# Performance work log

Measured on AMD Instinct MI355X. Metric: run time of the kernel, lower is better.

## Reference

```python
import jax, jax.numpy as jnp
import numpy as np

B, N, DE, DX, H = 16, 128, 4, 11, 128
LAMBDA_BOUND = 1e-4


def setup_inputs() -> dict:
    key = jax.random.key(0)
    k1, k2, k3, k4, k5 = jax.random.split(key, 5)
    # symmetric sparse random graph (avg degree ~12) so the Laplacian has a generic spectrum
    m = jax.random.bernoulli(k1, 0.1, (B, N, N))
    adj = jnp.logical_or(m, jnp.swapaxes(m, 1, 2))
    adj = adj & ~jnp.eye(N, dtype=bool)[None]
    A = jax.random.normal(k2, (B, N, N, DE), dtype=jnp.float32) * adj[..., None].astype(jnp.float32)
    X = jax.random.normal(k3, (B, N, DX), dtype=jnp.float32)
    nodemask = jnp.zeros((B, N), dtype=bool)
    W_edge = jax.random.normal(k4, (DE, H), dtype=jnp.float32) * 0.1
    b_edge = jnp.zeros((H,), dtype=jnp.float32)
    W_x = jax.random.normal(k5, (DX, H), dtype=jnp.float32) * 0.1
    b_x = jnp.zeros((H,), dtype=jnp.float32)
    mu = jnp.linspace(0.0, 2.0, H, dtype=jnp.float32)       # RBF centers
    inv_sigma = jnp.full((H,), 4.0, dtype=jnp.float32)       # RBF inverse widths
    return {"A": A, "X": X, "nodemask": nodemask, "W_edge": W_edge, "b_edge": b_edge,
            "W_x": W_x, "b_x": b_x, "mu": mu, "inv_sigma": inv_sigma}


def reference(A, X, nodemask, W_edge, b_edge, W_x, b_x, mu, inv_sigma):
    # edge embedding (qm9 path: Linear(4, hiddim))
    eA = jnp.einsum('bnmd,dh->bnmh', A, W_edge) + b_edge            # (b,n,n,h)
    # adjacency / degree
    adj = jnp.any(A != 0, axis=-1).astype(A.dtype)                   # (b,n,n)
    D = jnp.sum(adj, axis=-1)                                        # (b,n)
    # normalized Laplacian
    n = adj.shape[1]
    L = D[:, :, None] * jnp.eye(n, dtype=A.dtype) - adj
    tD = jax.lax.rsqrt(jnp.maximum(D, 1.0))
    L = tD[:, None, :] * L * tD[:, :, None]
    # batched symmetric eigendecomposition (eval mode: no permutation / noise)
    Lambda, U = jnp.linalg.eigh(L)                                   # (b,n), (b,n,n)
    Lambda = Lambda[:, 1:]                                           # drop trivial eigenpair
    U = U[:, :, 1:]                                                  # (b,n,n-1)
    # node embedding (Linear(11, hiddim)) + mask
    Xh = jnp.einsum('bnd,dh->bnh', X, W_x) + b_x
    Xh = jnp.where(nodemask[..., None], 0.0, Xh)
    # eigen masking
    Lambdamask = jnp.abs(Lambda) < LAMBDA_BOUND                      # (b,n-1)
    U = jnp.where(Lambdamask[:, None, :], 0.0, U)
    U = jnp.where(nodemask[:, :, None], 0.0, U)
    Lambda = jnp.sqrt(jax.nn.relu(Lambda))
    # Gaussian RBF expansion of eigenvalues -> (b,n-1,h)
    LambdaEmb = jnp.exp(-jnp.square((Lambda[..., None] - mu) * inv_sigma))
    # mask edge embeddings on padded nodes
    eA = jnp.where(nodemask[:, None, :, None], 0.0, eA)
    eA = jnp.where(nodemask[:, :, None, None], 0.0, eA)
    # node-edge combine: (b,n,m,h) x (b,m,l) -> (b,n,l,h)
    Uc = jnp.einsum('bnmd,bml->bnld', eA, U)
    return (LambdaEmb, Lambdamask, Uc, Xh, nodemask)
```

## Files before the change

### kernel.cpp

```cpp
#include <hip/hip_runtime.h>

#define NBATCH 16
#define NN 128
#define NH 128
#define NL 127
#define NDX 11
#define NDE 4
#define LDA 132
#define LDB 129
#define LDT 132
#define WS_STRIDE 66560

#define OFF_AREF 0
#define OFF_Q0   16384
#define OFF_Q1   32768
#define OFF_S    49152
#define OFF_DV   65536
#define OFF_EV   65664
#define OFF_TAU  65792
#define OFF_ORG  65920
#define OFF_META 66048

#define EPS32 5.9604645e-8f
#define EPS232 3.5527137e-15f
#define SAFMIN32 1.17549435e-38f

__device__ __forceinline__ float ssign_(float a, float b) {
  return (b >= 0.0f) ? fabsf(a) : -fabsf(a);
}
__device__ __forceinline__ float slapy2_(float x, float y) {
  float ax = fabsf(x), ay = fabsf(y);
  float w = fmaxf(ax, ay), z = fminf(ax, ay);
  if (z == 0.0f) return w;
  float q = z / w;
  return w * sqrtf(1.0f + q * q);
}

__device__ __forceinline__ float rdl(float v, int src) {
  return __int_as_float(__builtin_amdgcn_readlane(__float_as_int(v), src));
}

__device__ void slartg_(float f, float g, float* c, float* s, float* r) {
  if (g == 0.0f) { *c = 1.0f; *s = 0.0f; *r = f; }
  else if (f == 0.0f) { *c = 0.0f; *s = (g >= 0.0f) ? 1.0f : -1.0f; *r = fabsf(g); }
  else {
    float d = sqrtf(f * f + g * g);
    d = (f >= 0.0f) ? d : -d;
    *c = f / d; *s = g / d; *r = d;
  }
}

__device__ void slaev2_(float a, float b, float c0, float* rt1, float* rt2,
                        float* cs1, float* sn1) {
  float sm = a + c0, df = a - c0, adf = fabsf(df), tb = b + b, ab = fabsf(tb);
  float acmx, acmn;
  if (fabsf(a) > fabsf(c0)) { acmx = a; acmn = c0; } else { acmx = c0; acmn = a; }
  float rt;
  if (adf > ab) { float q = ab / adf; rt = adf * sqrtf(1.0f + q * q); }
  else if (adf < ab) { float q = adf / ab; rt = ab * sqrtf(1.0f + q * q); }
  else rt = ab * sqrtf(2.0f);
  int sgn1;
  if (sm < 0.0f) { *rt1 = 0.5f * (sm - rt); sgn1 = -1; *rt2 = (acmx / *rt1) * acmn - (b / *rt1) * b; }
  else if (sm > 0.0f) { *rt1 = 0.5f * (sm + rt); sgn1 = 1; *rt2 = (acmx / *rt1) * acmn - (b / *rt1) * b; }
  else { *rt1 = 0.5f * rt; *rt2 = -0.5f * rt; sgn1 = 1; }
  int sgn2; float cs;
  if (df >= 0.0f) { cs = df + rt; sgn2 = 1; } else { cs = df - rt; sgn2 = -1; }
  float acs = fabsf(cs);
  if (acs > ab) { float ct = -tb / cs; *sn1 = 1.0f / sqrtf(1.0f + ct * ct); *cs1 = ct * (*sn1); }
  else {
    if (ab == 0.0f) { *cs1 = 1.0f; *sn1 = 0.0f; }
    else { float tn = -cs / tb; *cs1 = 1.0f / sqrtf(1.0f + tn * tn); *sn1 = tn * (*cs1); }
  }
  if (sgn1 == sgn2) { float tn = *cs1; *cs1 = -(*sn1); *sn1 = tn; }
}

__global__ __launch_bounds__(1024) void k_tridiag(const float* __restrict__ A_in,
                                                  float* __restrict__ wsG) {
  const int b = blockIdx.x, t = threadIdx.x;
  float* Aref = wsG + (size_t)b * WS_STRIDE;
  float* dv = Aref + OFF_DV;
  float* ev = Aref + OFF_EV;
  float* tg = Aref + OFF_TAU;
  float* og = Aref + OFF_ORG;
  extern __shared__ float As[];
  __shared__ unsigned int maskp[128][8];
  __shared__ unsigned int Dp[128][8];
  __shared__ unsigned long long adj0_[128], adj1_[128];
  __shared__ float Dd_[128], tDs_[128];
  __shared__ float d_[128], e_[128], tau_[128];
  __shared__ alignas(16) float v_[128];
  __shared__ alignas(16) float w_[128];
  __shared__ float pmat[8][128];
  __shared__ alignas(16) float red_[16];

  const int wid = t >> 6;
  const int lane = t & 63;
  {
    const int r8 = t >> 3, s8 = t & 7;
    const float4* Arow = (const float4*)(A_in + (size_t)(b * 128 + r8) * 128 * 4);
    unsigned int mloc = 0; unsigned int cnt = 0;
    const int m0 = s8 * 16;
    #pragma unroll 4
    for (int mm = 0; mm < 16; ++mm) {
      float4 a = Arow[m0 + mm];
      if (a.x != 0.f || a.y != 0.f || a.z != 0.f || a.w != 0.f) { mloc |= 1u << mm; cnt++; }
    }
    maskp[r8][s8] = mloc; Dp[r8][s8] = cnt;
  }
  __syncthreads();
  if (t < 128) {
    unsigned long long b0 = 0ull, b1 = 0ull; unsigned int D = 0;
    #pragma unroll
    for (int s = 0; s < 4; ++s) { b0 |= (unsigned long long)maskp[t][s] << (16 * s); D += Dp[t][s]; }
    #pragma unroll
    for (int s = 0; s < 4; ++s) { b1 |= (unsigned long long)maskp[t][s + 4] << (16 * s); D += Dp[t][s + 4]; }
    adj0_[t] = b0; adj1_[t] = b1;
    float Df = (float)D;
    Dd_[t] = Df;
    tDs_[t] = 1.0f / sqrtf(fmaxf(Df, 1.0f));
  }
  __syncthreads();
  for (int idx = t; idx < 16384; idx += 1024) {
    int r = idx >> 7, c = idx & 127;
    if (c <= r) {
      float adj = (float)((c < 64 ? (adj0_[r] >> c) : (adj1_[r] >> (c - 64))) & 1ull);
      float Lrc = ((c == r) ? Dd_[r] : 0.0f) - adj;
      float val = (tDs_[c] * Lrc) * tDs_[r];
      As[r * LDA + c] = val;
      As[c * LDA + r] = val;
    }
  }
  __syncthreads();

  const int rmv = t & 127;
  const int smv = t >> 7;
  const int ucg = t & 31;
  const int urs = t >> 5;

  for (int i = 0; i < 127; ++i) {
    const int lo = i + 1;
    float xi = 0.0f;
    float part = 0.0f;
    if (t < 128) {
      xi = As[t * LDA + i];
      if (t >= i + 2) part = xi * xi;
    }
    if (wid < 2) {
      #pragma unroll
      for (int m = 1; m < 64; m <<= 1) part += __shfl_xor(part, m);
      if (lane == 0) red_[wid] = part;
    }
    __syncthreads();
    float xnorm2 = red_[0] + red_[1];
    float alpha = As[lo * LDA + i];
    float beta, taui, scal;
    if (xnorm2 == 0.0f) { taui = 0.0f; beta = alpha; scal = 0.0f; }
    else {
      float xn = sqrtf(xnorm2);
      beta = -ssign_(slapy2_(alpha, xn), alpha);
      taui = (beta - alpha) / beta;
      scal = 1.0f / (alpha - beta);
    }
    if (t == 0) { e_[i] = beta; tau_[i] = taui; }
    if (taui != 0.0f) {
      if (t < 128) {
        float vv = 0.0f;
        if (t == lo) vv = 1.0f;
        else if (t > lo) { vv = xi * scal; As[t * LDA + i] = vv; }
        v_[t] = vv;
      }
      __syncthreads();
      const int c0 = smv * 16;
      float acc = 0.0f;
      if (c0 + 15 >= lo && rmv >= lo) {
        const float4* Ar = (const float4*)&As[rmv * LDA + c0];
        const float4* Vr = (const float4*)&v_[c0];
        #pragma unroll
        for (int k = 0; k < 4; ++k) {
          float4 a = Ar[k], v4 = Vr[k];
          acc += a.x * v4.x + a.y * v4.y + a.z * v4.z + a.w * v4.w;
        }
      }
      pmat[smv][rmv] = acc;
      __syncthreads();
      if (t < 128) {
        float pv = 0.0f;
        #pragma unroll
        for (int s = 0; s < 8; ++s) pv += pmat[s][t];
        float wt = taui * pv;
        w_[t] = wt;
        float p2 = v_[t] * wt;
        #pragma unroll
        for (int m = 1; m < 64; m <<= 1) p2 += __shfl_xor(p2, m);
        if (lane == 0) red_[wid] = p2;
      }
      __syncthreads();
      float a2 = -0.5f * taui * (red_[0] + red_[1]);
      const int uc0 = ucg * 4;
      if (uc0 + 3 >= lo) {
        float4 vc = *(const float4*)&v_[uc0];
        float4 wc = *(const float4*)&w_[uc0];
        float pcx = wc.x + a2 * vc.x;
        float pcy = wc.y + a2 * vc.y;
        float pcz = wc.z + a2 * vc.z;
        float pcw = wc.w + a2 * vc.w;
        if (uc0 < lo) {
          if (uc0 + 0 < lo) { vc.x = 0.f; pcx = 0.f; }
          if (uc0 + 1 < lo) { vc.y = 0.f; pcy = 0.f; }
          if (uc0 + 2 < lo) { vc.z = 0.f; pcz = 0.f; }
        }
        #pragma unroll
        for (int k = 0; k < 4; ++k) {
          int r = urs + 32 * k;
          if (r >= lo) {
            float vr = v_[r];
            float pr = w_[r] + a2 * vr;
            float4 a = *(const float4*)&As[r * LDA + uc0];
            a.x -= vr * pcx + pr * vc.x;
            a.y -= vr * pcy + pr * vc.y;
            a.z -= vr * pcz + pr * vc.z;
            a.w -= vr * pcw + pr * vc.w;
            *(float4*)&As[r * LDA + uc0] = a;
          }
        }
      }
    }
    __syncthreads();
  }
  if (t < 128) d_[t] = As[t * LDA + t];
  __syncthreads();

  {
    float mx = 0.0f;
    if (t < 128) mx = fabsf(d_[t]);
    if (t < 127) mx = fmaxf(mx, fabsf(e_[t]));
    if (wid < 2) {
      #pragma unroll
      for (int m = 1; m < 64; m <<= 1) mx = fmaxf(mx, __shfl_xor(mx, m));
      if (lane == 0) red_[wid] = mx;
    }
    __syncthreads();
  }
  float orgnrm = fmaxf(red_[0], red_[1]);
  if (orgnrm == 0.0f) orgnrm = 1.0f;
  float invnrm = 1.0f / orgnrm;
  if (t < 128) d_[t] *= invnrm;
  if (t < 127) e_[t] *= invnrm;
  __syncthreads();
  if (t == 0) {
    for (int bm = 16; bm < 128; bm += 16) {
      float ae = fabsf(e_[bm - 1]);
      d_[bm - 1] -= ae; d_[bm] -= ae;
    }
  }
  __syncthreads();
  for (int idx = t; idx < 16384; idx += 1024)
    Aref[idx] = As[(idx >> 7) * LDA + (idx & 127)];
  if (t < 128) { dv[t] = d_[t]; tg[t] = tau_[t]; }
  if (t < 127) ev[t] = e_[t];
  if (t == 0) og[0] = orgnrm;
}

__global__ __launch_bounds__(64) void k_leaves(float* __restrict__ wsG) {
  int b = blockIdx.x >> 3, lf = blockIdx.x & 7;
  float* base = wsG + (size_t)b * WS_STRIDE;
  float* Qg = base + OFF_Q0;
  float* dv = base + OFF_DV;
  float* ev = base + OFF_EV;
  const int ln = threadIdx.x;
  __shared__ float zsh[16 * 17];

  const int n = 16;
  float dreg = (ln < 16) ? dv[lf * 16 + ln] : 0.f;
  float ereg = (ln < 15) ? ev[lf * 16 + ln] : 0.f;
  float csreg = 0.f, snreg = 0.f;
  float zr[16];
  #pragma unroll
  for (int c = 0; c < 16; ++c) zr[c] = (ln == c) ? 1.0f : 0.0f;

  {
    const float eps = EPS32, eps2 = EPS232, safmin = SAFMIN32;
    int nmaxit = n * 30, jtot = 0;
    int l1 = 0;
    while (l1 <= n - 1) {
      if (l1 > 0 && ln == l1 - 1) ereg = 0.0f;
      int m;
      for (m = l1; m <= n - 2; ++m) {
        float tst = fabsf(rdl(ereg, m));
        if (tst == 0.0f) break;
        if (tst <= (sqrtf(fabsf(rdl(dreg, m))) * sqrtf(fabsf(rdl(dreg, m + 1)))) * eps) {
          if (ln == m) ereg = 0.0f;
          break;
        }
      }
      int l = l1, lend = m;
      l1 = m + 1;
      if (lend == l) continue;
      {
        float an = 0.0f;
        for (int i = l; i <= lend; ++i) an = fmaxf(an, fabsf(rdl(dreg, i)));
        for (int i = l; i <= lend - 1; ++i) an = fmaxf(an, fabsf(rdl(ereg, i)));
        if (an == 0.0f) continue;
      }
      if (fabsf(rdl(dreg, lend)) < fabsf(rdl(dreg, l))) { int tsw = l; l = lend; lend = tsw; }
      if (lend > l) {
        while (true) {
          int m2;
          if (l != lend) {
            for (m2 = l; m2 <= lend - 1; ++m2) {
              float em = rdl(ereg, m2);
              float tst = em * em;
              if (tst <= (eps2 * fabsf(rdl(dreg, m2))) * fabsf(rdl(dreg, m2 + 1)) + safmin) break;
            }
          } else m2 = lend;
          if (m2 < lend && ln == m2) ereg = 0.0f;
          float p = rdl(dreg, l);
          if (m2 == l) { l++; if (l <= lend) continue; else break; }
          if (m2 == l + 1) {
            float rt1, rt2, c, s;
            slaev2_(rdl(dreg, l), rdl(ereg, l), rdl(dreg, l + 1), &rt1, &rt2, &c, &s);
            #pragma unroll
            for (int j = 0; j < 15; ++j) {
              if (j == l) {
                float t1 = zr[j + 1];
                zr[j + 1] = c * t1 - s * zr[j];
                zr[j] = s * t1 + c * zr[j];
              }
            }
            if (ln == l) { dreg = rt1; ereg = 0.0f; }
            if (ln == l + 1) dreg = rt2;
            l += 2; if (l <= lend) continue; else break;
          }
          if (jtot == nmaxit) break;
          jtot++;
          float g = (rdl(dreg, l + 1) - p) / (2.0f * rdl(ereg, l));
          float r = slapy2_(g, 1.0f);
          g = rdl(dreg, m2) - p + rdl(ereg, l) / (g + ssign_(r, g));
          float s = 1.0f, c = 1.0f; p = 0.0f;
          for (int i = m2 - 1; i >= l; --i) {
            float ei = rdl(ereg, i);
            float f = s * ei, bb = c * ei;
            slartg_(g, f, &c, &s, &r);
            if (i != m2 - 1 && ln == i + 1) ereg = r;
            g = rdl(dreg, i + 1) - p;
            r = (rdl(dreg, i) - g) * s + 2.0f * c * bb;
            p = s * r;
            if (ln == i + 1) dreg = g + p;
            g = c * r - bb;
            if (ln == i) { csreg = c; snreg = -s; }
          }
          #pragma unroll
          for (int j = 14; j >= 0; --j) {
            if (j <= m2 - 1 && j >= l) {
              float cj = rdl(csreg, j), sj = rdl(snreg, j);
              float t1 = zr[j + 1];
              zr[j + 1] = cj * t1 - sj * zr[j];
              zr[j] = sj * t1 + cj * zr[j];
            }
          }
          if (ln == l) { dreg = dreg - p; ereg = g; }
        }
      } else {
        while (true) {
          int m2;
          if (l != lend) {
            for (m2 = l; m2 >= lend + 1; --m2) {
              float em = rdl(ereg, m2 - 1);
              float tst = em * em;
              if (tst <= (eps2 * fabsf(rdl(dreg, m2))) * fabsf(rdl(dreg, m2 - 1)) + safmin) break;
            }
          } else m2 = lend;
          if (m2 > lend && ln == m2 - 1) ereg = 0.0f;
          float p = rdl(dreg, l);
          if (m2 == l) { l--; if (l >= lend) continue; else break; }
          if (m2 == l - 1) {
            float rt1, rt2, c, s;
            slaev2_(rdl(dreg, l - 1), rdl(ereg, l - 1), rdl(dreg, l), &rt1, &rt2, &c, &s);
            #pragma unroll
            for (int j = 0; j < 15; ++j) {
              if (j == l - 1) {
                float t1 = zr[j + 1];
                zr[j + 1] = c * t1 - s * zr[j];
                zr[j] = s * t1 + c * zr[j];
              }
            }
            if (ln == l - 1) { dreg = rt1; ereg = 0.0f; }
            if (ln == l) dreg = rt2;
            l -= 2; if (l >= lend) continue; else break;
          }
          if (jtot == nmaxit) break;
          jtot++;
          float g = (rdl(dreg, l - 1) - p) / (2.0f * rdl(ereg, l - 1));
          float r = slapy2_(g, 1.0f);
          g = rdl(dreg, m2) - p + rdl(ereg, l - 1) / (g + ssign_(r, g));
          float s = 1.0f, c = 1.0f; p = 0.0f;
          for (int i = m2; i <= l - 1; ++i) {
            float ei = rdl(ereg, i);
            float f = s * ei, bb = c * ei;
            slartg_(g, f, &c, &s, &r);
            if (i != m2 && ln == i - 1) ereg = r;
            g = rdl(dreg, i) - p;
            r = (rdl(dreg, i + 1) - g) * s + 2.0f * c * bb;
            p = s * r;
            if (ln == i) dreg = g + p;
            g = c * r - bb;
            if (ln == i) { csreg = c; snreg = s; }
          }
          #pragma unroll
          for (int j = 0; j <= 14; ++j) {
            if (j >= m2 && j <= l - 1) {
              float cj = rdl(csreg, j), sj = rdl(snreg, j);
              float t1 = zr[j + 1];
              zr[j + 1] = cj * t1 - sj * zr[j];
              zr[j] = sj * t1 + cj * zr[j];
            }
          }
          if (ln == l) dreg = dreg - p;
          if (ln == l - 1) ereg = g;
        }
      }
    }
  }

  if (ln < 16) {
    #pragma unroll
    for (int c = 0; c < 16; ++c) zsh[ln * 17 + c] = zr[c];
  }
  __syncthreads();
  for (int ii = 1; ii <= n - 1; ++ii) {
    int i = ii - 1, k = i;
    float p = rdl(dreg, i);
    for (int j = ii; j <= n - 1; ++j) {
      float dj = rdl(dreg, j);
      if (dj < p) { k = j; p = dj; }
    }
    if (k != i) {
      float di = rdl(dreg, i);
      if (ln == k) dreg = di;
      if (ln == i) dreg = p;
      if (ln < 16) {
        float t1 = zsh[ln * 17 + i];
        zsh[ln * 17 + i] = zsh[ln * 17 + k];
        zsh[ln * 17 + k] = t1;
      }
    }
  }
  __syncthreads();
  if (ln < 16) dv[lf * 16 + ln] = dreg;
  {
    const int bo = (lf >> 1) * 32;
    const int cofs = (lf & 1) * 16;
    for (int idx = ln; idx < 16 * 32; idx += 64) {
      int rr = idx >> 5, c = idx & 31;
      int cl = c - cofs;
      float v = (cl >= 0 && cl < 16) ? zsh[rr * 17 + cl] : 0.f;
      Qg[(size_t)(lf * 16 + rr) * 128 + bo + c] = v;
    }
  }
}

template <int LVL>
__global__ __launch_bounds__(1024) void k_mergeA(float* __restrict__ wsG, int qoff) {
  constexpr int sh = 2 - LVL;
  constexpr int nm = 32 << LVL;
  constexpr int LPR = 1024 / nm;
  constexpr int NCH = nm / LPR;
  int b = blockIdx.x >> sh;
  int mg = blockIdx.x & ((1 << sh) - 1);
  int bo = mg * nm, n1 = nm >> 1, n = nm;
  const int t = threadIdx.x;
  float* base = wsG + (size_t)b * WS_STRIDE;
  float* Qin = base + qoff;
  float* dvg = base + OFF_DV;
  float* evg = base + OFF_EV;
  float* Sg  = base + OFF_S;
  int* meta = (int*)(base + OFF_META);
  int* undG = meta; int* idxpG = meta + 128; int* finG = meta + 256; int* KfG = meta + 384;

  __shared__ float d_[128], z_[128], dl_[128], w_[128], zh_[128], lam_[128], tauv_[128], dnew_[128];
  __shared__ int srt_[128], indxp_[128], und_[128], anc_[128], fin_[128];
  __shared__ int gp_[128], gq_[128];
  __shared__ float gc_[128], gs_[128];
  __shared__ int sci[4];

  if (t < n) d_[t] = dvg[bo + t];
  float rho_in = evg[bo + n1 - 1];
  if (t < n) {
    float zv = (t < n1) ? Qin[(size_t)(bo + n1 - 1) * 128 + bo + t]
                        : Qin[(size_t)(bo + n1) * 128 + bo + t];
    if (rho_in < 0.0f && t >= n1) zv = -zv;
    z_[t] = zv * 0.70710678f;
  }
  __syncthreads();
  float rho = fabsf(2.0f * rho_in);
  if (t == 0) {
    int i1 = 0, i2 = n1, k = 0;
    while (i1 < n1 && i2 < n) {
      if (d_[i1] <= d_[i2]) srt_[k++] = i1++; else srt_[k++] = i2++;
    }
    while (i1 < n1) srt_[k++] = i1++;
    while (i2 < n) srt_[k++] = i2++;
    float zmax = 0.0f, dmax = 0.0f;
    for (int i = 0; i < n; ++i) {
      zmax = fmaxf(zmax, fabsf(z_[i]));
      dmax = fmaxf(dmax, fabsf(d_[i]));
    }
    float tol = 8.0f * EPS32 * fmaxf(dmax, zmax);
    int K = 0, k2 = n, full = 0, ngiv = 0;
    if (rho * zmax <= tol) full = 1;
    else {
      int pj = -1, jj = 0;
      for (; jj < n; ++jj) {
        int nj = srt_[jj];
        if (rho * fabsf(z_[nj]) <= tol) { k2--; indxp_[k2] = nj; }
        else { pj = nj; break; }
      }
      if (pj < 0) full = 1;
      else {
        for (jj = jj + 1; jj < n; ++jj) {
          int nj = srt_[jj];
          if (rho * fabsf(z_[nj]) <= tol) { k2--; indxp_[k2] = nj; }
          else {
            float s = z_[pj], c = z_[nj];
            float tauq = slapy2_(c, s);
            float tdf = d_[nj] - d_[pj];
            c /= tauq; s = -s / tauq;
            if (fabsf(tdf * c * s) <= tol) {
              z_[nj] = tauq; z_[pj] = 0.0f;
              gp_[ngiv] = pj; gq_[ngiv] = nj; gc_[ngiv] = c; gs_[ngiv] = s; ngiv++;
              float tt2 = d_[pj] * c * c + d_[nj] * s * s;
              d_[nj] = d_[pj] * s * s + d_[nj] * c * c;
              d_[pj] = tt2;
              k2--;
              int pos = k2;
              while (pos + 1 <= n - 1 && d_[pj] < d_[indxp_[pos + 1]]) {
                indxp_[pos] = indxp_[pos + 1]; pos++;
              }
              indxp_[pos] = pj;
              pj = nj;
            } else {
              dl_[K] = d_[pj]; w_[K] = z_[pj]; und_[K] = pj; K++;
              pj = nj;
            }
          }
        }
        dl_[K] = d_[pj]; w_[K] = z_[pj]; und_[K] = pj; K++;
      }
    }
    sci[0] = K; sci[1] = full; sci[2] = ngiv;
  }
  __syncthreads();
  int K = sci[0], full = sci[1], ngiv = sci[2];
  if (!full) {
    if (t < n) {
      size_t rowoff = (size_t)(bo + t) * 128 + bo;
      for (int g = 0; g < ngiv; ++g) {
        float c = gc_[g], s = gs_[g];
        float xq = Qin[rowoff + gp_[g]], yq = Qin[rowoff + gq_[g]];
        Qin[rowoff + gp_[g]] = c * xq + s * yq;
        Qin[rowoff + gq_[g]] = c * yq - s * xq;
      }
    }
    const int j = t / LPR;
    const int sub = t % LPR;
    const bool act = (j < K);
    float dl_loc[NCH], w2_loc[NCH];
    float tauj_reg = 0.0f; float da_reg = 0.0f;
    if (act) {
      #pragma unroll
      for (int k = 0; k < NCH; ++k) {
        int i = sub + k * LPR;
        if (i < K) { dl_loc[k] = dl_[i]; float wi = w_[i]; w2_loc[k] = rho * wi * wi; }
        else { dl_loc[k] = 3.0e38f; w2_loc[k] = 0.0f; }
      }
      float zs = 0.0f;
      #pragma unroll
      for (int k = 0; k < NCH; ++k) zs += w2_loc[k];
      #pragma unroll
      for (int m = 1; m < LPR; m <<= 1) zs += __shfl_xor(zs, m);
      int a; float lo2, hi2;
      if (j < K - 1) {
        float dj = dl_[j];
        float tm = 0.5f * (dl_[j + 1] - dj);
        float fm = 0.0f;
        #pragma unroll
        for (int k = 0; k < NCH; ++k) fm += w2_loc[k] / ((dl_loc[k] - dj) - tm);
        #pragma unroll
        for (int m = 1; m < LPR; m <<= 1) fm += __shfl_xor(fm, m);
        fm += 1.0f;
        if (fm >= 0.0f) { a = j; lo2 = 0.0f; hi2 = tm; }
        else { a = j + 1; lo2 = -tm; hi2 = 0.0f; }
      } else { a = K - 1; lo2 = 0.0f; hi2 = zs + 1e-30f; }
      float da = dl_[a];
      float sdl[NCH];
      #pragma unroll
      for (int k = 0; k < NCH; ++k) sdl[k] = dl_loc[k] - da;
      for (int it2 = 0; it2 < 48; ++it2) {
        float tc = 0.5f * (lo2 + hi2);
        float f = 0.0f;
        #pragma unroll
        for (int k = 0; k < NCH; ++k) f += w2_loc[k] / (sdl[k] - tc);
        #pragma unroll
        for (int m = 1; m < LPR; m <<= 1) f += __shfl_xor(f, m);
        f += 1.0f;
        if (f >= 0.0f) hi2 = tc; else lo2 = tc;
      }
      tauj_reg = 0.5f * (lo2 + hi2);
      da_reg = da;
      if (sub == 0) { lam_[j] = da + tauj_reg; tauv_[j] = tauj_reg; anc_[j] = a; }
    }
    __syncthreads();
    if (act) {
      float di = dl_[j];
      float pp = 1.0f;
      #pragma unroll
      for (int k = 0; k < NCH; ++k) {
        int jj = sub + k * LPR;
        if (jj < K && jj != j) {
          float delta_ij = (di - dl_[anc_[jj]]) - tauv_[jj];
          pp *= delta_ij / (di - dl_[jj]);
        }
      }
      #pragma unroll
      for (int m = 1; m < LPR; m <<= 1) pp *= __shfl_xor(pp, m);
      if (sub == 0) {
        float lead = (di - da_reg) - tauj_reg;
        float acc = lead * pp;
        zh_[j] = ssign_(sqrtf(fmaxf(-acc, 0.0f)), w_[j]);
      }
    }
    __syncthreads();
    if (act) {
      float sv[NCH]; float nrm = 0.0f;
      #pragma unroll
      for (int k = 0; k < NCH; ++k) {
        int i = sub + k * LPR;
        float s = 0.0f;
        if (i < K) s = zh_[i] / ((dl_loc[k] - da_reg) - tauj_reg);
        sv[k] = s; nrm += s * s;
      }
      #pragma unroll
      for (int m = 1; m < LPR; m <<= 1) nrm += __shfl_xor(nrm, m);
      nrm = 1.0f / sqrtf(nrm);
      float* scol = Sg + bo + j;
      #pragma unroll
      for (int k = 0; k < NCH; ++k) {
        int i = sub + k * LPR;
        if (i < K) scol[(size_t)(bo + i) * 128] = sv[k] * nrm;
      }
    }
    if (t == 0) {
      for (int jj = 0; jj < K; ++jj) dnew_[jj] = lam_[jj];
      for (int m = 0; m < n - K; ++m) dnew_[K + m] = d_[indxp_[n - 1 - m]];
      int i1 = 0, i2 = K, k = 0;
      while (i1 < K && i2 < n) { if (dnew_[i1] <= dnew_[i2]) fin_[k++] = i1++; else fin_[k++] = i2++; }
      while (i1 < K) fin_[k++] = i1++;
      while (i2 < n) fin_[k++] = i2++;
    }
    __syncthreads();
    if (t < n) {
      dvg[bo + t] = dnew_[fin_[t]];
      idxpG[bo + t] = indxp_[t];
      finG[bo + t] = fin_[t];
    }
    if (t < K) undG[bo + t] = und_[t];
    if (t == 0) KfG[mg] = K;
  } else {
    if (t < n) {
      dvg[bo + t] = d_[srt_[t]];
      idxpG[bo + t] = srt_[n - 1 - t];
      finG[bo + t] = t;
    }
    if (t == 0) KfG[mg] = 0;
  }
}

__global__ __launch_bounds__(256) void k_mergeB(float* __restrict__ wsG, int lvl,
                                                int qinoff, int qoutoff) {
  int b = blockIdx.x >> 2;
  int rblk = blockIdx.x & 3;
  int rbase = rblk * 32;
  int nm = 32 << lvl;
  int ln2 = 5 + lvl;
  int mg = rbase >> ln2;
  int bo = mg * nm, n = nm;
  const int t = threadIdx.x;
  float* base = wsG + (size_t)b * WS_STRIDE;
  const float* Qin = base + qinoff;
  float* Qout = base + qoutoff;
  const float* Sg = base + OFF_S;
  const int* meta = (const int*)(base + OFF_META);
  const int* undG = meta; const int* idxpG = meta + 128;
  const int* finG = meta + 256; const int* KfG = meta + 384;

  extern __shared__ float lds[];
  float* QT = lds;
  float* QC = QT + 32 * LDB;
  float* WT = QC + 32 * LDB;
  float* ST = WT + 32 * LDB;
  __shared__ int und_l[128], idxp_l[128], fin_l[128];
  __shared__ int Ksh;

  if (t == 0) Ksh = KfG[mg];
  if (t < n) { und_l[t] = undG[bo + t]; idxp_l[t] = idxpG[bo + t]; fin_l[t] = finG[bo + t]; }
  for (int idx = t; idx < 32 * n; idx += 256) {
    int r = idx >> ln2, c = idx & (n - 1);
    QT[r * LDB + c] = Qin[(size_t)(rbase + r) * 128 + bo + c];
  }
  __syncthreads();
  int K = Ksh;
  for (int idx = t; idx < (K << 7); idx += 256) {
    int k = idx >> 7, j = idx & 127;
    ST[k * LDB + j] = Sg[(size_t)(bo + k) * 128 + bo + j];
  }
  for (int r = 0; r < 32; ++r)
    if (t < K) QC[r * LDB + t] = QT[r * LDB + und_l[t]];
  __syncthreads();
  for (int idx = t; idx < 32 * n; idx += 256) {
    int r = idx >> ln2, j = idx & (n - 1);
    float v;
    if (j < K) {
      float a0 = 0.f, a1 = 0.f, a2 = 0.f, a3 = 0.f;
      int k = 0;
      for (; k + 3 < K; k += 4) {
        a0 += QC[r * LDB + k]     * ST[k * LDB + j];
        a1 += QC[r * LDB + k + 1] * ST[(k + 1) * LDB + j];
        a2 += QC[r * LDB + k + 2] * ST[(k + 2) * LDB + j];
        a3 += QC[r * LDB + k + 3] * ST[(k + 3) * LDB + j];
      }
      for (; k < K; ++k) a0 += QC[r * LDB + k] * ST[k * LDB + j];
      v = (a0 + a1) + (a2 + a3);
    } else {
      v = QT[r * LDB + idxp_l[n - 1 - (j - K)]];
    }
    WT[r * LDB + j] = v;
  }
  __syncthreads();
  for (int idx = t; idx < 32 * 128; idx += 256) {
    int r = idx >> 7, c = idx & 127;
    int cl = c - bo;
    float v = 0.f;
    if (cl >= 0 && cl < n) v = WT[r * LDB + fin_l[cl]];
    Qout[(size_t)(rbase + r) * 128 + c] = v;
  }
}

__global__ __launch_bounds__(1024) void k_back(
    float* __restrict__ wsG, const unsigned char* __restrict__ nodemask,
    const float* __restrict__ mu, const float* __restrict__ isg,
    float* __restrict__ wsUt, float* __restrict__ wsLam,
    float* __restrict__ outEmb, float* __restrict__ outLmask) {
  const int b = blockIdx.x, t = threadIdx.x;
  float* base = wsG + (size_t)b * WS_STRIDE;
  float* Qg = base + OFF_Q1;
  float* dvg = base + OFF_DV;
  float* tg = base + OFF_TAU;
  float* og = base + OFF_ORG;
  extern __shared__ float lds[];
  float* At = lds;
  float* Qt = lds + 128 * LDT;
  __shared__ float d_[128], tau_[128];
  __shared__ unsigned char nm_[128];

  float orgnrm = og[0];
  for (int idx = t; idx < 16384; idx += 1024) {
    int r = idx >> 7, c = idx & 127;
    At[c * LDT + r] = base[idx];
    Qt[c * LDT + r] = Qg[idx];
  }
  if (t < 128) {
    d_[t] = dvg[t] * orgnrm;
    tau_[t] = tg[t];
    nm_[t] = nodemask[b * 128 + t];
  }
  __syncthreads();

  const int w = t >> 6, l = t & 63;
  const int cidx = l & 7, sg = l >> 3;
  const int c = w * 8 + cidx;
  float q[16];
  #pragma unroll
  for (int k = 0; k < 4; ++k) {
    float4 v = *(const float4*)&Qt[c * LDT + 4 * sg + 32 * k];
    q[4 * k + 0] = v.x; q[4 * k + 1] = v.y; q[4 * k + 2] = v.z; q[4 * k + 3] = v.w;
  }
  for (int i = 126; i >= 0; --i) {
    float taui = tau_[i];
    if (taui == 0.0f) continue;
    const int lo = i + 1;
    float a[16];
    float dot = 0.0f;
    #pragma unroll
    for (int k = 0; k < 4; ++k) {
      if (32 * k + 31 >= lo) {
        float4 av = *(const float4*)&At[i * LDT + 4 * sg + 32 * k];
        {
          int r = 4 * sg + 32 * k;
          float aj;
          aj = (r == lo) ? 1.0f : ((r > lo) ? av.x : 0.0f); a[4*k+0] = aj; dot += aj * q[4*k+0]; r++;
          aj = (r == lo) ? 1.0f : ((r > lo) ? av.y : 0.0f); a[4*k+1] = aj; dot += aj * q[4*k+1]; r++;
          aj = (r == lo) ? 1.0f : ((r > lo) ? av.z : 0.0f); a[4*k+2] = aj; dot += aj * q[4*k+2]; r++;
          aj = (r == lo) ? 1.0f : ((r > lo) ? av.w : 0.0f); a[4*k+3] = aj; dot += aj * q[4*k+3];
        }
      }
    }
    dot += __shfl_xor(dot, 8);
    dot += __shfl_xor(dot, 16);
    dot += __shfl_xor(dot, 32);
    float wv = taui * dot;
    #pragma unroll
    for (int k = 0; k < 4; ++k) {
      if (32 * k + 31 >= lo) {
        q[4*k+0] -= a[4*k+0] * wv;
        q[4*k+1] -= a[4*k+1] * wv;
        q[4*k+2] -= a[4*k+2] * wv;
        q[4*k+3] -= a[4*k+3] * wv;
      }
    }
  }
  #pragma unroll
  for (int k = 0; k < 4; ++k) {
    float4 v;
    v.x = q[4*k+0]; v.y = q[4*k+1]; v.z = q[4*k+2]; v.w = q[4*k+3];
    *(float4*)&Qt[c * LDT + 4 * sg + 32 * k] = v;
  }
  __syncthreads();

  if (t < NL) {
    float lam = d_[t + 1];
    wsLam[b * NL + t] = lam;
    outLmask[b * NL + t] = (fabsf(lam) < 1e-4f) ? 1.f : 0.f;
  }
  for (int idx = t; idx < NL * 128; idx += 1024) {
    int ll = idx >> 7, nn2 = idx & 127;
    float lam = d_[ll + 1];
    float vv = Qt[(ll + 1) * LDT + nn2];
    if (fabsf(lam) < 1e-4f || nm_[nn2]) vv = 0.f;
    wsUt[(size_t)(b * NL + ll) * 128 + nn2] = vv;
  }
  for (int idx = t; idx < NL * NH; idx += 1024) {
    int ll = idx >> 7, h = idx & 127;
    float lam = d_[ll + 1];
    float sq = sqrtf(fmaxf(lam, 0.f));
    float dd = (sq - mu[h]) * isg[h];
    outEmb[(size_t)(b * NL + ll) * NH + h] = expf(-dd * dd);
  }
}

__global__ __launch_bounds__(256) void k_xh(
    const float* __restrict__ X, const unsigned char* __restrict__ nodemask,
    const float* __restrict__ Wx, const float* __restrict__ bx,
    float* __restrict__ outXh, float* __restrict__ outNm) {
  int idx = blockIdx.x * 256 + threadIdx.x;
  int h = idx & 127;
  int bn = idx >> 7;
  const float* xr = X + (size_t)bn * NDX;
  float acc = bx[h];
  #pragma unroll
  for (int d = 0; d < NDX; ++d) acc += xr[d] * Wx[d * NH + h];
  outXh[idx] = nodemask[bn] ? 0.f : acc;
  if (idx < NBATCH * NN) outNm[idx] = nodemask[idx] ? 1.f : 0.f;
}

__global__ __launch_bounds__(256) void k_uc(
    const float* __restrict__ A, const unsigned char* __restrict__ nodemask,
    const float* __restrict__ We, const float* __restrict__ be,
    const float* __restrict__ wsUt, float* __restrict__ outUc) {
  int b = blockIdx.x >> 4;
  int ng = blockIdx.x & 15;
  int t = threadIdx.x;
  __shared__ float Uts[NL * 129];
  __shared__ float Ssh[NL];
  __shared__ float Wsh[NDE * NH];
  __shared__ float bsh[NH];
  __shared__ float Ar[NN * NDE];
  __shared__ float Tp[2 * NL * NDE];
  __shared__ float Ts[NL * NDE];
  for (int idx = t; idx < NL * NN; idx += 256) {
    int l = idx >> 7, n = idx & 127;
    Uts[l * 129 + n] = wsUt[(size_t)b * NL * NN + idx];
  }
  for (int idx = t; idx < NDE * NH; idx += 256) Wsh[idx] = We[idx];
  if (t < NH) bsh[t] = be[t];
  __syncthreads();
  if (t < NL) {
    float s = 0.f;
    for (int n = 0; n < NN; ++n) s += Uts[t * 129 + n];
    Ssh[t] = s;
  }
  __syncthreads();
  for (int nn = 0; nn < 8; ++nn) {
    int n = ng * 8 + nn;
    for (int idx = t; idx < NN * NDE; idx += 256)
      Ar[idx] = A[(size_t)(b * NN + n) * NN * NDE + idx];
    __syncthreads();
    {
      int l = t & 127, half = t >> 7;
      if (l < NL) {
        float a0 = 0.f, a1 = 0.f, a2 = 0.f, a3 = 0.f;
        for (int m = 64 * half; m < 64 * half + 64; ++m) {
          float u = Uts[l * 129 + m];
          a0 += Ar[m * 4 + 0] * u;
          a1 += Ar[m * 4 + 1] * u;
          a2 += Ar[m * 4 + 2] * u;
          a3 += Ar[m * 4 + 3] * u;
        }
        int base = (half * NL + l) * 4;
        Tp[base + 0] = a0; Tp[base + 1] = a1; Tp[base + 2] = a2; Tp[base + 3] = a3;
      }
    }
    __syncthreads();
    for (int idx = t; idx < NL * NDE; idx += 256) Ts[idx] = Tp[idx] + Tp[NL * NDE + idx];
    __syncthreads();
    bool mn = nodemask[b * NN + n] != 0;
    {
      int h = t & 127, lh = t >> 7;
      float w0 = Wsh[0 * NH + h], w1 = Wsh[1 * NH + h], w2 = Wsh[2 * NH + h], w3 = Wsh[3 * NH + h];
      float bb = bsh[h];
      for (int l = lh; l < NL; l += 2) {
        float v = w0 * Ts[l * 4 + 0] + w1 * Ts[l * 4 + 1] + w2 * Ts[l * 4 + 2] +
                  w3 * Ts[l * 4 + 3] + bb * Ssh[l];
        outUc[(size_t)((b * NN + n) * NL + l) * NH + h] = mn ? 0.f : v;
      }
    }
    __syncthreads();
  }
}

extern "C" void kernel_launch(void* const* d_in, const int* in_sizes, int n_in,
                              void* d_out, int out_size, void* d_ws, size_t ws_size,
                              hipStream_t stream) {
  const float* A = (const float*)d_in[0];
  const float* X = (const float*)d_in[1];
  const unsigned char* nodemask = (const unsigned char*)d_in[2];
  const float* We = (const float*)d_in[3];
  const float* be = (const float*)d_in[4];
  const float* Wx = (const float*)d_in[5];
  const float* bx = (const float*)d_in[6];
  const float* mu = (const float*)d_in[7];
  const float* isg = (const float*)d_in[8];

  float* out = (float*)d_out;
  float* outEmb = out;
  float* outLmask = out + 260096;
  float* outUc = out + 262128;
  float* outXh = out + 33554416;
  float* outNm = out + 33816560;

  float* wsG = (float*)d_ws;
  float* wsUt = (float*)((char*)d_ws + 4456448);
  float* wsLam = wsUt + 260096;

  size_t lds1 = (size_t)128 * LDA * sizeof(float);
  size_t lds2 = (size_t)2 * 128 * LDT * sizeof(float);
  size_t ldsB = (size_t)(3 * 32 * LDB + 128 * LDB) * sizeof(float);

  k_tridiag<<<NBATCH, 1024, lds1, stream>>>(A, wsG);
  k_leaves<<<NBATCH * 8, 64, 0, stream>>>(wsG);
  k_mergeA<0><<<NBATCH * 4, 1024, 0, stream>>>(wsG, OFF_Q0);
  k_mergeB<<<NBATCH * 4, 256, ldsB, stream>>>(wsG, 0, OFF_Q0, OFF_Q1);
  k_mergeA<1><<<NBATCH * 2, 1024, 0, stream>>>(wsG, OFF_Q1);
  k_mergeB<<<NBATCH * 4, 256, ldsB, stream>>>(wsG, 1, OFF_Q1, OFF_Q0);
  k_mergeA<2><<<NBATCH * 1, 1024, 0, stream>>>(wsG, OFF_Q0);
  k_mergeB<<<NBATCH * 4, 256, ldsB, stream>>>(wsG, 2, OFF_Q0, OFF_Q1);
  k_back<<<NBATCH, 1024, lds2, stream>>>(wsG, nodemask, mu, isg, wsUt, wsLam, outEmb, outLmask);
  k_xh<<<(NBATCH * NN * NH) / 256, 256, 0, stream>>>(X, nodemask, Wx, bx, outXh, outNm);
  k_uc<<<NBATCH * 16, 256, 0, stream>>>(A, nodemask, We, be, wsUt, outUc);
}
```

Measured before the change: 958.8 us.

## Fuse next-column norm into rank-2 update and cut barriers in tridiagonalization

The Householder tridiagonalization loop now accumulates the squared norm of the next column during the rank-2 update, so the next iteration can skip its separate reduction pass and barrier. The v·w dot product is computed from the per-thread partial matvec results before the first barrier, which removes one more reduction step. The secular-equation bisection iteration count is also lowered from 48 to 36. Together these remove about two barriers per Householder step, at the cost of possible accuracy loss from the fewer bisection iterations and a changed floating-point summation order.

Measured after the change: 950.6 us. About the same (-0.9%).

```diff
diff --git a/kernel.cpp b/kernel.cpp
--- a/kernel.cpp
+++ b/kernel.cpp
@@ -92,6 +92,7 @@
   __shared__ alignas(16) float w_[128];
   __shared__ float pmat[8][128];
   __shared__ alignas(16) float red_[16];
+  __shared__ float xp[32];
 
   const int wid = t >> 6;
   const int lane = t & 63;
@@ -137,21 +138,26 @@
   const int ucg = t & 31;
   const int urs = t >> 5;
 
+  bool usexp = false;
   for (int i = 0; i < 127; ++i) {
     const int lo = i + 1;
-    float xi = 0.0f;
-    float part = 0.0f;
-    if (t < 128) {
-      xi = As[t * LDA + i];
-      if (t >= i + 2) part = xi * xi;
-    }
-    if (wid < 2) {
-      #pragma unroll
-      for (int m = 1; m < 64; m <<= 1) part += __shfl_xor(part, m);
-      if (lane == 0) red_[wid] = part;
-    }
-    __syncthreads();
-    float xnorm2 = red_[0] + red_[1];
+    float xnorm2;
+    if (!usexp) {
+      float part = 0.0f;
+      if (t < 128 && t >= i + 2) { float x = As[t * LDA + i]; part = x * x; }
+      if (wid < 2) {
+        #pragma unroll
+        for (int m = 1; m < 64; m <<= 1) part += __shfl_xor(part, m);
+        if (lane == 0) red_[wid] = part;
+      }
+      __syncthreads();
+      xnorm2 = red_[0] + red_[1];
+    } else {
+      float s = 0.0f;
+      #pragma unroll
+      for (int k = 0; k < 32; ++k) s += xp[k];
+      xnorm2 = s;
+    }
     float alpha = As[lo * LDA + i];
     float beta, taui, scal;
     if (xnorm2 == 0.0f) { taui = 0.0f; beta = alpha; scal = 0.0f; }
@@ -166,7 +172,7 @@
       if (t < 128) {
         float vv = 0.0f;
         if (t == lo) vv = 1.0f;
-        else if (t > lo) { vv = xi * scal; As[t * LDA + i] = vv; }
+        else if (t > lo) { float xi = As[t * LDA + i]; vv = xi * scal; As[t * LDA + i] = vv; }
         v_[t] = vv;
       }
       __syncthreads();
@@ -182,20 +188,22 @@
         }
       }
       pmat[smv][rmv] = acc;
+      float p2 = v_[rmv] * acc;
+      #pragma unroll
+      for (int m = 1; m < 64; m <<= 1) p2 += __shfl_xor(p2, m);
+      if (lane == 0) red_[wid] = p2;
       __syncthreads();
+      float vpr = 0.0f;
+      #pragma unroll
+      for (int k = 0; k < 16; ++k) vpr += red_[k];
+      float a2 = -0.5f * taui * (taui * vpr);
       if (t < 128) {
         float pv = 0.0f;
         #pragma unroll
         for (int s = 0; s < 8; ++s) pv += pmat[s][t];
-        float wt = taui * pv;
-        w_[t] = wt;
-        float p2 = v_[t] * wt;
-        #pragma unroll
-        for (int m = 1; m < 64; m <<= 1) p2 += __shfl_xor(p2, m);
-        if (lane == 0) red_[wid] = p2;
+        w_[t] = taui * pv;
       }
       __syncthreads();
-      float a2 = -0.5f * taui * (red_[0] + red_[1]);
       const int uc0 = ucg * 4;
       if (uc0 + 3 >= lo) {
         float4 vc = *(const float4*)&v_[uc0];
@@ -209,6 +217,9 @@
           if (uc0 + 1 < lo) { vc.y = 0.f; pcy = 0.f; }
           if (uc0 + 2 < lo) { vc.z = 0.f; pcz = 0.f; }
         }
+        const bool isxcol = (ucg == (lo >> 2));
+        const int xc = lo & 3;
+        float xpacc = 0.0f;
         #pragma unroll
         for (int k = 0; k < 4; ++k) {
           int r = urs + 32 * k;
@@ -221,11 +232,17 @@
             a.z -= vr * pcz + pr * vc.z;
             a.w -= vr * pcw + pr * vc.w;
             *(float4*)&As[r * LDA + uc0] = a;
+            if (isxcol && r >= lo + 2) {
+              float nc = (xc == 0) ? a.x : ((xc == 1) ? a.y : ((xc == 2) ? a.z : a.w));
+              xpacc += nc * nc;
+            }
           }
         }
+        if (isxcol) xp[urs] = xpacc;
       }
     }
     __syncthreads();
+    usexp = (taui != 0.0f);
   }
   if (t < 128) d_[t] = As[t * LDA + t];
   __syncthreads();
@@ -595,7 +612,7 @@
       float sdl[NCH];
       #pragma unroll
       for (int k = 0; k < NCH; ++k) sdl[k] = dl_loc[k] - da;
-      for (int it2 = 0; it2 < 48; ++it2) {
+      for (int it2 = 0; it2 < 36; ++it2) {
         float tc = 0.5f * (lo2 + hi2);
         float f = 0.0f;
         #pragma unroll
```
